# Optimization experiments

Hardware: AMD Instinct MI355X
Metric: run time of the kernel (lower is better)

Reference implementation:

```python
import jax, jax.numpy as jnp
import numpy as np
import math

N_NODES = 20000
N_EDGES = 640000
N_BASIS = 10
NUM_NEIGHBORS = 32.0


def _fctp_scalar_attr(x0, x1, attr, W0, W1):
    """FullyConnectedTensorProduct(irreps_in, '0e' attr) == per-irrep linear
    scaled by the scalar attribute, with e3nn fan-in normalization.
    x0: [N, mul0] scalars, x1: [N, mul1, 3] vectors, attr: [N, 1]."""
    a = attr[:, :1]
    y0 = (x0 * a) @ W0 / jnp.sqrt(jnp.asarray(W0.shape[0], x0.dtype))
    y1 = jnp.einsum('nui,uv->nvi', x1 * a[:, :, None], W1) / jnp.sqrt(jnp.asarray(W1.shape[0], x1.dtype))
    return y0, y1


def setup_inputs() -> dict:
    key = jax.random.key(0)
    ks = jax.random.split(key, 13)
    node_input = jax.random.normal(ks[0], (N_NODES, 80), jnp.float32)
    node_attr = jnp.ones((N_NODES, 1), jnp.float32)
    edge_attr = jax.random.normal(ks[1], (N_EDGES, 4), jnp.float32)
    edge_scalars = jax.random.uniform(ks[2], (N_EDGES, N_BASIS), jnp.float32)
    edge_index = jax.random.randint(ks[3], (2, N_EDGES), 0, N_NODES)
    # learned params
    W_sc0 = jax.random.normal(ks[4], (32, 32), jnp.float32)
    W_sc1 = jax.random.normal(ks[5], (16, 16), jnp.float32)
    W_l1_0 = jax.random.normal(ks[6], (32, 32), jnp.float32)
    W_l1_1 = jax.random.normal(ks[7], (16, 16), jnp.float32)
    W_fc0 = jax.random.normal(ks[8], (N_BASIS, 64), jnp.float32)
    W_fc1 = jax.random.normal(ks[9], (64, 96), jnp.float32)  # 96 = tp.weight_numel
    W_l2_0 = jax.random.normal(ks[10], (48, 32), jnp.float32)
    W_l2_1 = jax.random.normal(ks[11], (48, 16), jnp.float32)
    return dict(node_input=node_input, node_attr=node_attr, edge_attr=edge_attr,
                edge_scalars=edge_scalars, W_sc0=W_sc0, W_sc1=W_sc1,
                W_l1_0=W_l1_0, W_l1_1=W_l1_1, W_fc0=W_fc0, W_fc1=W_fc1,
                W_l2_0=W_l2_0, W_l2_1=W_l2_1, edge_index=edge_index)


def reference(node_input, node_attr, edge_attr, edge_scalars,
              W_sc0, W_sc1, W_l1_0, W_l1_1, W_fc0, W_fc1, W_l2_0, W_l2_1,
              edge_index):
    N = node_input.shape[0]
    x0 = node_input[:, :32]                     # 32x0e
    x1 = node_input[:, 32:].reshape(N, 16, 3)   # 16x1o

    # self-connection and pre-TP linear
    s0, s1 = _fctp_scalar_attr(x0, x1, node_attr, W_sc0, W_sc1)
    y0, y1 = _fctp_scalar_attr(x0, x1, node_attr, W_l1_0, W_l1_1)

    # radial MLP -> per-edge TP weights (e3nn FullyConnectedNet: no bias, fan-in norm, silu)
    h = jax.nn.silu(edge_scalars @ W_fc0 / jnp.sqrt(jnp.asarray(N_BASIS, jnp.float32)))
    w = h @ W_fc1 / jnp.sqrt(jnp.asarray(64.0, jnp.float32))  # [E, 96]
    w_a, w_b, w_c, w_d = w[:, :32], w[:, 32:64], w[:, 64:80], w[:, 80:96]

    src, dst = edge_index[0], edge_index[1]
    xs0 = y0[src]                               # [E, 32]
    xs1 = y1[src]                               # [E, 16, 3]
    e0 = edge_attr[:, :1]                       # [E, 1] 0e sh
    e1 = edge_attr[:, 1:4]                      # [E, 3] 1o sh

    # 'uvu' tensor product paths -> irreps_mid = 32x0e + 16x0e + 32x1o + 16x1o
    m_a = w_a * xs0 * e0                                    # 0e x 0e -> 0e  [E,32]
    m_b = (w_b * xs0)[:, :, None] * e1[:, None, :]          # 0e x 1o -> 1o  [E,32,3]
    m_c = w_c[:, :, None] * xs1 * e0[:, :, None]            # 1o x 0e -> 1o  [E,16,3]
    m_d = w_d * jnp.einsum('eui,ei->eu', xs1, e1) / jnp.sqrt(jnp.asarray(3.0, jnp.float32))  # 1o x 1o -> 0e [E,16]
    mid0 = jnp.concatenate([m_a, m_d], axis=1)              # [E, 48] scalars
    mid1 = jnp.concatenate([m_b, m_c], axis=1)              # [E, 48, 3] vectors

    # scatter-add into destination nodes, normalized by sqrt(num_neighbors)
    inv = 1.0 / jnp.sqrt(jnp.asarray(NUM_NEIGHBORS, jnp.float32))
    agg0 = jax.ops.segment_sum(mid0, dst, num_segments=N) * inv
    agg1 = jax.ops.segment_sum(mid1, dst, num_segments=N) * inv

    # lin2: FCTP(irreps_mid, '0e') -> irreps_out, attr == 1
    z0 = agg0 @ W_l2_0 / jnp.sqrt(jnp.asarray(48.0, jnp.float32))
    z1 = jnp.einsum('nui,uv->nvi', agg1, W_l2_1) / jnp.sqrt(jnp.asarray(48.0, jnp.float32))

    # skip mix: output_mask of sc is all ones here (all out irreps reachable)
    c_s = math.sin(math.pi / 8)
    c_x = math.cos(math.pi / 8)
    out0 = c_s * s0 + c_x * z0
    out1 = c_s * s1 + c_x * z1
    return jnp.concatenate([out0, out1.reshape(N, 48)], axis=1)
```

## Files before the change

kernel.cpp:

```cpp
#include <hip/hip_runtime.h>

#define N_NODES 20000
#define N_EDGES 640000
#define N_MT (N_EDGES/16)

typedef short short8 __attribute__((ext_vector_type(8)));
typedef float f32x4 __attribute__((ext_vector_type(4)));

__device__ __forceinline__ unsigned int f2bf(float x){
  unsigned int u = __builtin_bit_cast(unsigned int, x);
  u += 0x7fffu + ((u >> 16) & 1u);
  return u >> 16;
}
__device__ __forceinline__ float bf2f(unsigned short u){
  unsigned int v = ((unsigned int)u) << 16;
  return __builtin_bit_cast(float, v);
}
__device__ __forceinline__ float bflo(unsigned int u){
  return __builtin_bit_cast(float, u << 16);
}
__device__ __forceinline__ float bfhi(unsigned int u){
  return __builtin_bit_cast(float, u & 0xffff0000u);
}

__device__ __forceinline__ void wave_lds_fence(){
  __asm__ volatile("s_waitcnt lgkmcnt(0)" ::: "memory");
}

#define HIST_BLOCKS 625
#define YN_BLOCKS   (N_NODES/16)
#define AGGZ_BLOCKS 938

__global__ void k_pre(const int* __restrict__ ei, int* __restrict__ counts,
                      const float* __restrict__ ni, const float* __restrict__ na,
                      const float* __restrict__ Wl10, const float* __restrict__ Wl11,
                      unsigned short* __restrict__ y, float4* __restrict__ aggz){
  if (blockIdx.x < HIST_BLOCKS){
    int i = blockIdx.x*256 + threadIdx.x;
    if (i < N_EDGES/4){
      int4 d4 = *(const int4*)(ei + N_EDGES + i*4);
      atomicAdd(&counts[d4.x], 1);
      atomicAdd(&counts[d4.y], 1);
      atomicAdd(&counts[d4.z], 1);
      atomicAdd(&counts[d4.w], 1);
    }
    return;
  }
  if (blockIdx.x >= HIST_BLOCKS + YN_BLOCKS){
    int i = (blockIdx.x - HIST_BLOCKS - YN_BLOCKS)*256 + threadIdx.x;
    if (i < 240000){
      float4 z = {0.f,0.f,0.f,0.f};
      float4* p = aggz + (size_t)i*4;
      p[0]=z; p[1]=z; p[2]=z; p[3]=z;
    }
    return;
  }
  __shared__ float sW0[1024];
  __shared__ float sW1[256];
  __shared__ float sni[16*84];
  __shared__ float sna[16];
  const int t = threadIdx.x;
  const int nb = (blockIdx.x - HIST_BLOCKS)*16;
  for (int i=t; i<1024; i+=256) sW0[i] = Wl10[i];
  if (t < 256) sW1[t] = Wl11[t];
  for (int i=t; i<320; i+=256){
    int n = i/20, q = i - n*20;
    *(float4*)&sni[n*84 + q*4] = *(const float4*)(ni + (size_t)(nb+n)*80 + q*4);
  }
  if (t < 16) sna[t] = na[nb + t];
  __syncthreads();
  for (int i=t; i<1280; i+=256){
    int n = i/80, k = i - n*80;
    const float* row = sni + n*84;
    float a = sna[n];
    float acc = 0.f;
    if (k < 32){
      #pragma unroll
      for (int u=0; u<32; ++u) acc += row[u]*sW0[u*32+k];
      y[(size_t)nb*80 + i] = (unsigned short)f2bf(acc * a * 0.17677669529663687f);
    } else {
      int kk = k-32, v = kk/3, ii = kk - v*3;
      #pragma unroll
      for (int u=0; u<16; ++u) acc += row[32+u*3+ii]*sW1[u*16+v];
      y[(size_t)nb*80 + i] = (unsigned short)f2bf(acc * a * 0.25f);
    }
  }
}

__global__ void k_alloc(const int* __restrict__ counts, int* __restrict__ ctr,
                        int* __restrict__ cursor){
  __shared__ int wsum[4];
  __shared__ int s_base;
  const int t = threadIdx.x;
  const int lane = t & 63, wv = t >> 6;
  const int n = blockIdx.x*256 + t;
  int v = (n < N_NODES) ? counts[n] : 0;
  int x = v;
  #pragma unroll
  for (int off=1; off<64; off<<=1){
    int sh = __shfl_up(x, off, 64);
    if (lane >= off) x += sh;
  }
  if (lane == 63) wsum[wv] = x;
  __syncthreads();
  if (t == 0){
    int s0 = wsum[0], s1 = wsum[1], s2 = wsum[2], s3 = wsum[3];
    int total = s0 + s1 + s2 + s3;
    wsum[0] = 0; wsum[1] = s0; wsum[2] = s0+s1; wsum[3] = s0+s1+s2;
    s_base = atomicAdd(ctr, total);
  }
  __syncthreads();
  if (n < N_NODES) cursor[n] = s_base + wsum[wv] + (x - v);
}

__global__ void k_fill(const int* __restrict__ ei, const float* __restrict__ ea,
                       const float* __restrict__ es, int* __restrict__ cursor,
                       uint4* __restrict__ meta){
  int e = blockIdx.x*256 + threadIdx.x;
  if (e >= N_EDGES) return;
  int s = ei[e], d = ei[N_EDGES + e];
  int pos = atomicAdd(&cursor[d], 1);
  const float* eap = ea + (size_t)e*4;
  const float* esp = es + (size_t)e*10;
  unsigned int u0 = f2bf(esp[0]) | (f2bf(esp[1])<<16);
  unsigned int u1 = f2bf(esp[2]) | (f2bf(esp[3])<<16);
  unsigned int u2 = f2bf(esp[4]) | (f2bf(esp[5])<<16);
  unsigned int u3 = f2bf(esp[6]) | (f2bf(esp[7])<<16);
  unsigned int u4 = f2bf(esp[8]) | (f2bf(esp[9])<<16);
  unsigned int u5 = f2bf(eap[0]) | (f2bf(eap[1])<<16);
  unsigned int u6 = f2bf(eap[2]) | (f2bf(eap[3])<<16);
  unsigned int u7 = ((unsigned int)s << 16) | (unsigned int)d;
  uint4* mp = meta + (size_t)pos*2;
  mp[0] = make_uint4(u0,u1,u2,u3);
  mp[1] = make_uint4(u4,u5,u6,u7);
}

__global__ __launch_bounds__(256) void k_edge(
    const uint2* __restrict__ meta,
    const float* __restrict__ Wfc0, const float* __restrict__ Wfc1,
    const unsigned short* __restrict__ yb, float* __restrict__ agg){
  __shared__ float s_wfc0[640];
  __shared__ unsigned short s_w[4][16*98];
  __shared__ unsigned short s_y[4][16*88];
  __shared__ float s_m[4][16*20];

  const int t = threadIdx.x;
  const int w = t >> 6, l = t & 63;
  const int r = l & 15, part = l >> 4;
  const int q = l & 3;

  for (int i = t; i < 640; i += 256) s_wfc0[i] = Wfc0[i];

  short8 b0[6], b1[6];
  #pragma unroll
  for (int nt=0; nt<6; ++nt){
    #pragma unroll
    for (int j=0; j<8; ++j){
      b0[nt][j] = (short)f2bf(Wfc1[(     part*8+j)*96 + nt*16 + r]);
      b1[nt][j] = (short)f2bf(Wfc1[(32 + part*8+j)*96 + nt*16 + r]);
    }
  }
  __syncthreads();

  int o_c[3], yo[3], eai[3];
  #pragma unroll
  for (int p=0; p<3; ++p){
    int c = p*64 + l;
    if (c < 32)      { o_c[p]=c;    yo[p]=c;        eai[p]=0; }
    else if (c < 48) { int u=c-32;  o_c[p]=80+u;    yo[p]=32+3*u; eai[p]=0; }
    else if (c < 144){ int idx=c-48;  int u=idx/3, fi=idx-u*3; o_c[p]=32+u; yo[p]=u;        eai[p]=1+fi; }
    else             { int idx=c-144; int u=idx/3, i =idx-u*3; o_c[p]=64+u; yo[p]=32+3*u+i; eai[p]=0; }
  }
  const bool dot0 = (l >= 32) && (l < 48);

  unsigned short* sw = s_w[w];
  unsigned short* sy = s_y[w];
  float* sm = s_m[w];

  const int o0 = (part==0) ? 0 : (part==1) ? 24 : (part==2) ? 40 : 64;
  const bool has3 = (part & 1) == 0;

  const int gw = blockIdx.x*4 + w;
  const int nw = gridDim.x*4;
  const int m0 = (int)(((long long)gw     * N_MT) / nw);
  const int m1 = (int)(((long long)(gw+1) * N_MT) / nw);
  if (m0 >= m1) return;

  uint2 mreg = meta[(size_t)m0*64 + l];

  float acc0 = 0.f, acc1 = 0.f, acc2 = 0.f;
  int dcur = -1;

  for (int m = m0; m < m1; ++m){
    const int mnx = (m+1 < m1) ? (m+1) : m;
    uint2 mnext = meta[(size_t)mnx*64 + l];

    const int packed = __shfl((int)mreg.y, 4*r + 3);
    const int isrc = ((unsigned int)packed) >> 16;
    const int idst = packed & 0xffff;

    {
      const unsigned short* yrow = yb + (size_t)isrc*80;
      uint4 va = *(const uint4*)(yrow + o0);
      uint4 vb = *(const uint4*)(yrow + o0 + 8);
      uint4 vc;
      if (has3) vc = *(const uint4*)(yrow + o0 + 16);
      unsigned short* syr = sy + r*88;
      *(uint4*)(syr + o0)      = va;
      *(uint4*)(syr + o0 + 8)  = vb;
      if (has3) *(uint4*)(syr + o0 + 16) = vc;
    }
    {
      float* sme = sm + (l>>2)*20;
      float f0 = bflo(mreg.x), f1 = bfhi(mreg.x);
      float f2 = bflo(mreg.y), f3 = bfhi(mreg.y);
      if (q == 0){
        sme[4]=f0; sme[5]=f1; sme[6]=f2; sme[7]=f3;
      } else if (q == 1){
        sme[8]=f0; sme[9]=f1; sme[10]=f2; sme[11]=f3;
      } else if (q == 2){
        sme[12]=f0; sme[13]=f1; sme[0]=f2; sme[1]=f3;
      } else {
        sme[2]=f0; sme[3]=f1;
      }
    }
    wave_lds_fence();

    const float* esr = sm + r*20 + 4;
    float hv0[8], hv1[8];
    #pragma unroll
    for (int j=0; j<8; ++j){ hv0[j]=0.f; hv1[j]=0.f; }
    #pragma unroll
    for (int k=0; k<10; ++k){
      float ev = esr[k];
      const float* wr = s_wfc0 + k*64 + part*8;
      #pragma unroll
      for (int j=0; j<8; ++j){ hv0[j] += ev*wr[j]; hv1[j] += ev*wr[32+j]; }
    }
    short8 a0, a1;
    #pragma unroll
    for (int j=0; j<8; ++j){
      float x0 = hv0[j]*0.31622776601683794f;
      float x1 = hv1[j]*0.31622776601683794f;
      a0[j] = (short)f2bf(x0/(1.f+__expf(-x0)));
      a1[j] = (short)f2bf(x1/(1.f+__expf(-x1)));
    }

    #pragma unroll
    for (int nt=0; nt<6; ++nt){
      f32x4 acc = {0.f,0.f,0.f,0.f};
      acc = __builtin_amdgcn_mfma_f32_16x16x32_bf16(a0, b0[nt], acc, 0,0,0);
      acc = __builtin_amdgcn_mfma_f32_16x16x32_bf16(a1, b1[nt], acc, 0,0,0);
      #pragma unroll
      for (int rr=0; rr<4; ++rr)
        sw[(part*4+rr)*98 + nt*16 + r] = (unsigned short)f2bf(acc[rr]*0.125f);
    }
    wave_lds_fence();

    for (int e=0; e<16; ++e){
      int de = __shfl(idst, e);
      if (de != dcur){
        if (dcur >= 0){
          unsafeAtomicAdd(&agg[(size_t)dcur*192 +       l], acc0);
          unsafeAtomicAdd(&agg[(size_t)dcur*192 +  64 + l], acc1);
          unsafeAtomicAdd(&agg[(size_t)dcur*192 + 128 + l], acc2);
        }
        acc0 = acc1 = acc2 = 0.f;
        dcur = de;
      }
      const float* sme = sm + e*20;
      const unsigned short* swe = sw + e*98;
      const unsigned short* sye = sy + e*88;
      float m0v;
      if (dot0){
        m0v = bf2f(swe[o_c[0]]) *
              (bf2f(sye[yo[0]])*sme[1] + bf2f(sye[yo[0]+1])*sme[2] + bf2f(sye[yo[0]+2])*sme[3])
              * 0.5773502691896258f;
      } else {
        m0v = bf2f(swe[o_c[0]]) * bf2f(sye[yo[0]]) * sme[eai[0]];
      }
      acc0 += m0v;
      acc1 += bf2f(swe[o_c[1]]) * bf2f(sye[yo[1]]) * sme[eai[1]];
      acc2 += bf2f(swe[o_c[2]]) * bf2f(sye[yo[2]]) * sme[eai[2]];
    }
    wave_lds_fence();

    mreg = mnext;
  }
  if (dcur >= 0){
    unsafeAtomicAdd(&agg[(size_t)dcur*192 +       l], acc0);
    unsafeAtomicAdd(&agg[(size_t)dcur*192 +  64 + l], acc1);
    unsafeAtomicAdd(&agg[(size_t)dcur*192 + 128 + l], acc2);
  }
}

__global__ void k_finish(const float* __restrict__ ni, const float* __restrict__ na,
    const float* __restrict__ Wsc0, const float* __restrict__ Wsc1,
    const float* __restrict__ Wl20, const float* __restrict__ Wl21,
    const float* __restrict__ agg, float* __restrict__ out){
  __shared__ float sWsc0[1024];
  __shared__ float sWsc1[256];
  __shared__ float sWl20[1536];
  __shared__ float sWl21[768];
  __shared__ float sni[16*84];
  __shared__ float sag[16*196];
  __shared__ float sna[16];
  const int t = threadIdx.x;
  const int nb = blockIdx.x*16;
  for (int i=t; i<1024; i+=256) sWsc0[i] = Wsc0[i];
  if (t < 256) sWsc1[t] = Wsc1[t];
  for (int i=t; i<1536; i+=256) sWl20[i] = Wl20[i];
  for (int i=t; i<768;  i+=256) sWl21[i] = Wl21[i];
  for (int i=t; i<320;  i+=256){
    int n = i/20, q = i - n*20;
    *(float4*)&sni[n*84 + q*4] = *(const float4*)(ni + (size_t)(nb+n)*80 + q*4);
  }
  for (int i=t; i<768;  i+=256){
    int n = i/48, q = i - n*48;
    *(float4*)&sag[n*196 + q*4] = *(const float4*)(agg + (size_t)(nb+n)*192 + q*4);
  }
  if (t < 16) sna[t] = na[nb + t];
  __syncthreads();

  const float c_s = 0.3826834323650898f;
  const float c_x = 0.9238795325112867f;
  const float zscale = 0.17677669529663687f * 0.14433756729740643f;
  for (int i=t; i<1280; i+=256){
    int n = i/80, k = i - n*80;
    const float* row = sni + n*84;
    const float* ag  = sag + n*196;
    float a = sna[n];
    float s = 0.f, z = 0.f;
    if (k < 32){
      #pragma unroll
      for (int u=0; u<32; ++u) s += row[u]*sWsc0[u*32+k];
      s *= a * 0.17677669529663687f;
      #pragma unroll
      for (int u=0; u<48; ++u) z += ag[u]*sWl20[u*32+k];
    } else {
      int kk=k-32, v=kk/3, ii=kk-v*3;
      #pragma unroll
      for (int u=0; u<16; ++u) s += row[32+u*3+ii]*sWsc1[u*16+v];
      s *= a * 0.25f;
      #pragma unroll
      for (int u=0; u<48; ++u) z += ag[48+u*3+ii]*sWl21[u*16+v];
    }
    out[(size_t)nb*80 + i] = c_s*s + c_x*z*zscale;
  }
}

extern "C" void kernel_launch(void* const* d_in, const int* in_sizes, int n_in,
                              void* d_out, int out_size, void* d_ws, size_t ws_size,
                              hipStream_t stream){
  const float* node_input   = (const float*)d_in[0];
  const float* node_attr    = (const float*)d_in[1];
  const float* edge_attr    = (const float*)d_in[2];
  const float* edge_scalars = (const float*)d_in[3];
  const float* W_sc0 = (const float*)d_in[4];
  const float* W_sc1 = (const float*)d_in[5];
  const float* W_l1_0 = (const float*)d_in[6];
  const float* W_l1_1 = (const float*)d_in[7];
  const float* W_fc0 = (const float*)d_in[8];
  const float* W_fc1 = (const float*)d_in[9];
  const float* W_l2_0 = (const float*)d_in[10];
  const float* W_l2_1 = (const float*)d_in[11];
  const int* edge_index = (const int*)d_in[12];
  float* out = (float*)d_out;

  char* ws = (char*)d_ws;
  unsigned short* y = (unsigned short*)ws;
  float*  agg    = (float*)(ws + 3200000);
  int*    counts = (int*)(ws + 18560000);
  int*    ctr    = (int*)(ws + 18640000);
  int*    cursor = (int*)(ws + 18640064);
  uint4*  meta   = (uint4*)(ws + 18722048);

  hipMemsetAsync(counts, 0, 80064, stream);

  k_pre  <<<HIST_BLOCKS + YN_BLOCKS + AGGZ_BLOCKS, 256, 0, stream>>>(
            edge_index, counts, node_input, node_attr, W_l1_0, W_l1_1,
            y, (float4*)agg);
  k_alloc<<<(N_NODES+255)/256, 256, 0, stream>>>(counts, ctr, cursor);
  k_fill <<<(N_EDGES+255)/256, 256, 0, stream>>>(edge_index, edge_attr, edge_scalars,
                                                 cursor, meta);
  k_edge <<<1280, 256, 0, stream>>>((const uint2*)meta, W_fc0, W_fc1, y, agg);
  k_finish<<<YN_BLOCKS, 256, 0, stream>>>(node_input, node_attr, W_sc0, W_sc1,
                                          W_l2_0, W_l2_1, agg, out);
}
```

Before: 337.4 us.

## Double-buffer source-row gathers into LDS via direct global-to-LDS loads in edge kernel

The edge kernel now gathers each tile's source-node rows straight into a double-buffered LDS area with global_load_lds, issued one tile ahead, and stores the packed bf16 edge metadata raw in LDS instead of unpacking it to floats. Destination indices are read from LDS rather than shuffled, and the grid drops from 1280 to 768 blocks. The aim is to hide gather latency behind the MLP/MFMA work of the current tile and cut VGPR and LDS unpacking traffic. In exchange LDS use per block grows, the per-iteration vmcnt(0) wait can stall on the prefetch, and fewer blocks give less parallelism.

Result: faster. 322.3 us (-4.5%).

```diff
diff --git a/kernel.cpp b/kernel.cpp
--- a/kernel.cpp
+++ b/kernel.cpp
@@ -16,15 +16,19 @@
   unsigned int v = ((unsigned int)u) << 16;
   return __builtin_bit_cast(float, v);
 }
-__device__ __forceinline__ float bflo(unsigned int u){
-  return __builtin_bit_cast(float, u << 16);
-}
-__device__ __forceinline__ float bfhi(unsigned int u){
-  return __builtin_bit_cast(float, u & 0xffff0000u);
-}
 
 __device__ __forceinline__ void wave_lds_fence(){
   __asm__ volatile("s_waitcnt lgkmcnt(0)" ::: "memory");
+}
+__device__ __forceinline__ void wave_vm_fence(){
+  __asm__ volatile("s_waitcnt vmcnt(0)" ::: "memory");
+}
+
+__device__ __forceinline__ void gload16(const void* g, void* l){
+  __builtin_amdgcn_global_load_lds(
+      (const __attribute__((address_space(1))) unsigned int*)g,
+      (__attribute__((address_space(3))) unsigned int*)l,
+      16, 0, 0);
 }
 
 #define HIST_BLOCKS 625
@@ -140,14 +144,13 @@
     const float* __restrict__ Wfc0, const float* __restrict__ Wfc1,
     const unsigned short* __restrict__ yb, float* __restrict__ agg){
   __shared__ float s_wfc0[640];
-  __shared__ unsigned short s_w[4][16*98];
-  __shared__ unsigned short s_y[4][16*88];
-  __shared__ float s_m[4][16*20];
+  __shared__ __align__(16) unsigned short s_w[4][16*98];
+  __shared__ __align__(16) unsigned short s_y[4][2][16*96];
+  __shared__ __align__(16) unsigned int  s_m[4][2][16*8];
 
   const int t = threadIdx.x;
   const int w = t >> 6, l = t & 63;
   const int r = l & 15, part = l >> 4;
-  const int q = l & 3;
 
   for (int i = t; i < 640; i += 256) s_wfc0[i] = Wfc0[i];
 
@@ -174,11 +177,14 @@
   const bool dot0 = (l >= 32) && (l < 48);
 
   unsigned short* sw = s_w[w];
-  unsigned short* sy = s_y[w];
-  float* sm = s_m[w];
-
-  const int o0 = (part==0) ? 0 : (part==1) ? 24 : (part==2) ? 40 : 64;
-  const bool has3 = (part & 1) == 0;
+
+  int row_i[3], cir_i[3];
+  #pragma unroll
+  for (int i=0; i<3; ++i){
+    int idx = i*64 + l;
+    row_i[i] = idx/12;
+    cir_i[i] = (idx - 12*row_i[i])*16;
+  }
 
   const int gw = blockIdx.x*4 + w;
   const int nw = gridDim.x*4;
@@ -187,52 +193,51 @@
   if (m0 >= m1) return;
 
   uint2 mreg = meta[(size_t)m0*64 + l];
+  {
+    unsigned short* syn = s_y[w][0];
+    #pragma unroll
+    for (int i=0; i<3; ++i){
+      int pk = __shfl((int)mreg.y, 4*row_i[i] + 3);
+      unsigned src = ((unsigned)pk) >> 16;
+      gload16((const char*)yb + (size_t)src*160 + cir_i[i], (char*)syn + i*1024);
+    }
+    *(uint2*)(&s_m[w][0][(l>>2)*8 + (l&3)*2]) = mreg;
+  }
+  mreg = meta[(size_t)((m0+1 < m1) ? m0+1 : m1-1)*64 + l];
 
   float acc0 = 0.f, acc1 = 0.f, acc2 = 0.f;
   int dcur = -1;
+  int b = 0;
 
   for (int m = m0; m < m1; ++m){
-    const int mnx = (m+1 < m1) ? (m+1) : m;
-    uint2 mnext = meta[(size_t)mnx*64 + l];
-
-    const int packed = __shfl((int)mreg.y, 4*r + 3);
-    const int isrc = ((unsigned int)packed) >> 16;
-    const int idst = packed & 0xffff;
-
+    wave_vm_fence();
+    const int nb2 = b ^ 1;
     {
-      const unsigned short* yrow = yb + (size_t)isrc*80;
-      uint4 va = *(const uint4*)(yrow + o0);
-      uint4 vb = *(const uint4*)(yrow + o0 + 8);
-      uint4 vc;
-      if (has3) vc = *(const uint4*)(yrow + o0 + 16);
-      unsigned short* syr = sy + r*88;
-      *(uint4*)(syr + o0)      = va;
-      *(uint4*)(syr + o0 + 8)  = vb;
-      if (has3) *(uint4*)(syr + o0 + 16) = vc;
+      unsigned short* syn = s_y[w][nb2];
+      #pragma unroll
+      for (int i=0; i<3; ++i){
+        int pk = __shfl((int)mreg.y, 4*row_i[i] + 3);
+        unsigned src = ((unsigned)pk) >> 16;
+        gload16((const char*)yb + (size_t)src*160 + cir_i[i], (char*)syn + i*1024);
+      }
+      *(uint2*)(&s_m[w][nb2][(l>>2)*8 + (l&3)*2]) = mreg;
     }
     {
-      float* sme = sm + (l>>2)*20;
-      float f0 = bflo(mreg.x), f1 = bfhi(mreg.x);
-      float f2 = bflo(mreg.y), f3 = bfhi(mreg.y);
-      if (q == 0){
-        sme[4]=f0; sme[5]=f1; sme[6]=f2; sme[7]=f3;
-      } else if (q == 1){
-        sme[8]=f0; sme[9]=f1; sme[10]=f2; sme[11]=f3;
-      } else if (q == 2){
-        sme[12]=f0; sme[13]=f1; sme[0]=f2; sme[1]=f3;
-      } else {
-        sme[2]=f0; sme[3]=f1;
-      }
+      int mnx = (m+2 < m1) ? m+2 : m1-1;
+      mreg = meta[(size_t)mnx*64 + l];
     }
     wave_lds_fence();
 
-    const float* esr = sm + r*20 + 4;
+    const unsigned int* smu = s_m[w][b];
+    const unsigned short* syb = s_y[w][b];
+
+    const unsigned short* esr = (const unsigned short*)(smu + r*8);
     float hv0[8], hv1[8];
     #pragma unroll
     for (int j=0; j<8; ++j){ hv0[j]=0.f; hv1[j]=0.f; }
     #pragma unroll
     for (int k=0; k<10; ++k){
-      float ev = esr[k];
+      float ev = bf2f(esr[k]);
       const float* wr = s_wfc0 + k*64 + part*8;
       #pragma unroll
       for (int j=0; j<8; ++j){ hv0[j] += ev*wr[j]; hv1[j] += ev*wr[32+j]; }
@@ -258,7 +263,7 @@
     wave_lds_fence();
 
     for (int e=0; e<16; ++e){
-      int de = __shfl(idst, e);
+      int de = (int)(smu[e*8 + 7] & 0xffffu);
       if (de != dcur){
         if (dcur >= 0){
           unsafeAtomicAdd(&agg[(size_t)dcur*192 +       l], acc0);
@@ -268,24 +273,24 @@
         acc0 = acc1 = acc2 = 0.f;
         dcur = de;
       }
-      const float* sme = sm + e*20;
+      const unsigned short* sme = (const unsigned short*)(smu + e*8);
       const unsigned short* swe = sw + e*98;
-      const unsigned short* sye = sy + e*88;
+      const unsigned short* sye = syb + e*96;
       float m0v;
       if (dot0){
         m0v = bf2f(swe[o_c[0]]) *
-              (bf2f(sye[yo[0]])*sme[1] + bf2f(sye[yo[0]+1])*sme[2] + bf2f(sye[yo[0]+2])*sme[3])
+              (bf2f(sye[yo[0]])*bf2f(sme[11]) + bf2f(sye[yo[0]+1])*bf2f(sme[12])
+               + bf2f(sye[yo[0]+2])*bf2f(sme[13]))
               * 0.5773502691896258f;
       } else {
-        m0v = bf2f(swe[o_c[0]]) * bf2f(sye[yo[0]]) * sme[eai[0]];
+        m0v = bf2f(swe[o_c[0]]) * bf2f(sye[yo[0]]) * bf2f(sme[10 + eai[0]]);
       }
       acc0 += m0v;
-      acc1 += bf2f(swe[o_c[1]]) * bf2f(sye[yo[1]]) * sme[eai[1]];
-      acc2 += bf2f(swe[o_c[2]]) * bf2f(sye[yo[2]]) * sme[eai[2]];
-    }
-    wave_lds_fence();
-
-    mreg = mnext;
+      acc1 += bf2f(swe[o_c[1]]) * bf2f(sye[yo[1]]) * bf2f(sme[10 + eai[1]]);
+      acc2 += bf2f(swe[o_c[2]]) * bf2f(sye[yo[2]]) * bf2f(sme[10 + eai[2]]);
+    }
+
+    b = nb2;
   }
   if (dcur >= 0){
     unsafeAtomicAdd(&agg[(size_t)dcur*192 +       l], acc0);
@@ -383,7 +388,7 @@
   k_alloc<<<(N_NODES+255)/256, 256, 0, stream>>>(counts, ctr, cursor);
   k_fill <<<(N_EDGES+255)/256, 256, 0, stream>>>(edge_index, edge_attr, edge_scalars,
                                                  cursor, meta);
-  k_edge <<<1280, 256, 0, stream>>>((const uint2*)meta, W_fc0, W_fc1, y, agg);
+  k_edge <<<768, 256, 0, stream>>>((const uint2*)meta, W_fc0, W_fc1, y, agg);
   k_finish<<<YN_BLOCKS, 256, 0, stream>>>(node_input, node_attr, W_sc0, W_sc1,
                                           W_l2_0, W_l2_1, agg, out);
 }
```
